# Performance work log

Measured on AMD Instinct MI355X. Metric: run time of the kernel, lower is better.

The kernel has to match this reference:

```python
import jax, jax.numpy as jnp
import numpy as np

HIDDEN = 1024
INNER = 2048  # hidden * expand_factor
STATE = 64
K = 4  # conv kernel size
BATCH, SEQ = 2, 2048


def setup_inputs() -> dict:
    key = jax.random.key(0)
    ks = jax.random.split(key, 8)
    def w(k, shape, scale=0.02):
        return (jax.random.normal(k, shape, jnp.float32) * scale)
    return {
        "x": jax.random.normal(ks[0], (BATCH, SEQ, HIDDEN), jnp.float32),
        "W_in": w(ks[1], (HIDDEN, 2 * INNER)),
        "conv_w": w(ks[2], (INNER, 1, K), 0.2),   # depthwise conv kernel [O, I/groups=1, K]
        "conv_b": jnp.zeros((INNER,), jnp.float32),
        "W_dt": w(ks[3], (INNER, INNER)),
        "b_dt": jnp.linspace(-4.0, -2.0, INNER).astype(jnp.float32),  # log(exp(linspace)) = linspace
        "W_B": w(ks[4], (INNER, STATE)),
        "W_C": w(ks[5], (INNER, STATE)),
        "D": jnp.ones((INNER,), jnp.float32),
        "W_out": w(ks[6], (INNER, HIDDEN)),
    }


def reference(x, W_in, conv_w, conv_b, W_dt, b_dt, W_B, W_C, D, W_out):
    batch, seq_len, _ = x.shape
    inner = W_dt.shape[0]
    state_dim = W_B.shape[1]

    # input projection and gate split
    xz = x @ W_in                              # [B, L, 2*inner]
    x_inner, z = jnp.split(xz, 2, axis=-1)

    # causal depthwise conv1d (pad both sides by K-1 then truncate == left-pad K-1)
    xc = jnp.transpose(x_inner, (0, 2, 1))    # [B, inner, L]
    k = conv_w.shape[-1]
    xc = jax.lax.conv_general_dilated(
        xc, conv_w, window_strides=(1,), padding=[(k - 1, 0)],
        dimension_numbers=("NCH", "OIH", "NCH"), feature_group_count=inner)
    xc = xc + conv_b[None, :, None]
    xc = jax.nn.silu(jnp.transpose(xc, (0, 2, 1)))   # [B, L, inner]

    # selective SSM parameters
    dt = jax.nn.softplus(xc @ W_dt + b_dt)    # [B, L, inner]
    Bm = xc @ W_B                             # [B, L, N]
    Cm = xc @ W_C                             # [B, L, N]
    a = jnp.exp(-dt)                          # [B, L, inner]
    dtx = dt * xc                             # [B, L, inner]

    # sequential selective scan over time: state[B, inner, N]
    def step(state, inp):
        a_t, dtx_t, b_t, c_t = inp
        state = a_t[..., None] * state + dtx_t[..., None] * b_t[:, None, :]
        y_t = jnp.einsum("bin,bn->bi", state, c_t)
        return state, y_t

    init = jnp.zeros((batch, inner, state_dim), x.dtype)
    xs = (jnp.swapaxes(a, 0, 1), jnp.swapaxes(dtx, 0, 1),
          jnp.swapaxes(Bm, 0, 1), jnp.swapaxes(Cm, 0, 1))
    _, ys = jax.lax.scan(step, init, xs)      # ys: [L, B, inner]
    y = jnp.swapaxes(ys, 0, 1) + D * xc       # skip connection

    y = y * jax.nn.silu(z)                    # output gate
    return y @ W_out                          # [B, L, hidden]
```

## Files before the change

### kernel.cpp

```cpp
#include <hip/hip_runtime.h>
#include <hip/hip_bf16.h>
#include <math.h>

#define BATCH  2
#define SEQ    2048
#define HID    1024
#define INNER  2048
#define NSTATE 64
#define NTOK   (BATCH * SEQ)
#define TCHUNK 64
#define NCHUNK (SEQ / TCHUNK)
#define NMID   (INNER + 2 * NSTATE)
#define LDH    1056
#define LDI    2080

typedef __bf16 bf16x8 __attribute__((ext_vector_type(8)));
typedef float  f32x4  __attribute__((ext_vector_type(4)));

typedef const __attribute__((address_space(1))) char* gas_ptr;
typedef __attribute__((address_space(3))) char*       las_ptr;

__device__ __forceinline__ void gload16(const void* g, void* l) {
  __builtin_amdgcn_global_load_lds((gas_ptr)g, (las_ptr)l, 16, 0, 0);
}

__device__ __forceinline__ unsigned short f2bf(float f) {
  __hip_bfloat16 h = __float2bfloat16(f);
  return __builtin_bit_cast(unsigned short, h);
}
__device__ __forceinline__ float bf2f(unsigned short u) {
  unsigned int x = ((unsigned int)u) << 16;
  return __builtin_bit_cast(float, x);
}

__global__ __launch_bounds__(256) void cvt_pad_kernel(
    const float* __restrict__ in, __hip_bfloat16* __restrict__ out, int n4) {
  int i = blockIdx.x * 256 + threadIdx.x;
  if (i >= n4) return;
  const int r = i >> 8;
  const int c = (i & 255) * 4;
  float4 v = *(const float4*)&in[(size_t)r * HID + c];
  ushort4 u;
  u.x = f2bf(v.x); u.y = f2bf(v.y); u.z = f2bf(v.z); u.w = f2bf(v.w);
  *(ushort4*)&out[(size_t)r * LDH + c] = u;
}

__global__ __launch_bounds__(256) void transpose_cvt_kernel(
    const float* __restrict__ in, __hip_bfloat16* __restrict__ out,
    int R, int C, int ostride) {
  __shared__ float tile[32][33];
  int tx = threadIdx.x & 31, ty = threadIdx.x >> 5;
  int c0 = blockIdx.x * 32, r0 = blockIdx.y * 32;
#pragma unroll
  for (int i = 0; i < 4; ++i)
    tile[ty + 8 * i][tx] = in[(size_t)(r0 + ty + 8 * i) * C + c0 + tx];
  __syncthreads();
#pragma unroll
  for (int i = 0; i < 4; ++i)
    out[(size_t)(c0 + ty + 8 * i) * ostride + r0 + tx] =
        __float2bfloat16(tile[tx][ty + 8 * i]);
}

template <int EPI>
__global__ __launch_bounds__(256, 4) void gemm_bt_kernel(
    const __hip_bfloat16* __restrict__ A, const __hip_bfloat16* __restrict__ Bt,
    int M, int N, int Klen, int ldk, int gridN, int nwg, int mnwg,
    float* __restrict__ Cout, int ldc, int ldo,
    __hip_bfloat16* __restrict__ o0, __hip_bfloat16* __restrict__ o1) {
  __shared__ __align__(16) __hip_bfloat16 As[128 * 64];
  __shared__ __align__(16) __hip_bfloat16 Bs[128 * 64];
  const int tid = threadIdx.x;
  const int lane = tid & 63;
  const int w = tid >> 6;
  const int wr = w >> 1, wc = w & 1;

  const int orig = blockIdx.x;
  const int q8 = nwg >> 3, r8 = nwg & 7;
  const int xcd = orig & 7, seq = orig >> 3;
  const int wg = (xcd < r8 ? xcd * (q8 + 1) : r8 * (q8 + 1) + (xcd - r8) * q8) + seq;
  const int kz = wg / mnwg;
  const int wgr = wg - kz * mnwg;
  const int m0 = (wgr / gridN) * 128;
  const int n0 = (wgr % gridN) * 128;

  const __hip_bfloat16* Ab = A + (size_t)kz * Klen;
  const __hip_bfloat16* Bb = Bt + (size_t)kz * Klen;

  f32x4 acc[4][4];
#pragma unroll
  for (int i = 0; i < 4; ++i)
#pragma unroll
    for (int j = 0; j < 4; ++j)
#pragma unroll
      for (int r2 = 0; r2 < 4; ++r2) acc[i][j][r2] = 0.f;

  const int g8row = lane >> 3;
  const int scol = ((lane & 7) ^ g8row) * 8;
  const __hip_bfloat16* Agp = Ab + (size_t)(m0 + w * 32 + g8row) * ldk + scol;
  const __hip_bfloat16* Bgp = Bb + (size_t)(n0 + w * 32 + g8row) * ldk + scol;
  __hip_bfloat16* lA = As + (w * 32) * 64;
  __hip_bfloat16* lB = Bs + (w * 32) * 64;

  const int lrow = lane & 15, lk = lane >> 4;
  const int arow0 = wr * 64 + lrow;
  const int brow0 = wc * 64 + lrow;

  const int nt = Klen >> 6;
  for (int t = 0; t < nt; ++t) {
    __syncthreads();
#pragma unroll
    for (int g = 0; g < 4; ++g) {
      gload16(Agp + (size_t)(g * 8) * ldk + t * 64, lA + (g * 8) * 64);
      gload16(Bgp + (size_t)(g * 8) * ldk + t * 64, lB + (g * 8) * 64);
    }
    __syncthreads();
#pragma unroll
    for (int ss = 0; ss < 2; ++ss) {
      bf16x8 af[4], bv[4];
#pragma unroll
      for (int i = 0; i < 4; ++i) {
        const int ra = arow0 + i * 16;
        af[i] = *(const bf16x8*)(As + ra * 64 + (((ss * 4 + lk) ^ (ra & 7)) * 8));
        const int rb = brow0 + i * 16;
        bv[i] = *(const bf16x8*)(Bs + rb * 64 + (((ss * 4 + lk) ^ (rb & 7)) * 8));
      }
#pragma unroll
      for (int i = 0; i < 4; ++i)
#pragma unroll
        for (int j = 0; j < 4; ++j)
          acc[i][j] = __builtin_amdgcn_mfma_f32_16x16x32_bf16(af[i], bv[j], acc[i][j], 0, 0, 0);
    }
  }

#pragma unroll
  for (int i = 0; i < 4; ++i) {
#pragma unroll
    for (int j = 0; j < 4; ++j) {
#pragma unroll
      for (int r2 = 0; r2 < 4; ++r2) {
        const int row = m0 + wr * 64 + i * 16 + lk * 4 + r2;
        const int col = n0 + wc * 64 + j * 16 + lrow;
        const float v = acc[i][j][r2];
        if constexpr (EPI == 0) {
          Cout[(size_t)kz * M * ldc + (size_t)row * ldc + col] = v;
        } else if constexpr (EPI == 1) {
          if (col < INNER) o0[(size_t)row * ldo + col] = __float2bfloat16(v);
          else             o1[(size_t)row * ldo + (col - INNER)] = __float2bfloat16(v);
        } else {
          o0[(size_t)kz * M * ldc + (size_t)row * ldc + col] = __float2bfloat16(v);
        }
      }
    }
  }
}

__global__ __launch_bounds__(256) void reduce_mid_kernel(
    const __hip_bfloat16* __restrict__ P, const float* __restrict__ bdt,
    const __hip_bfloat16* __restrict__ xch, unsigned int* __restrict__ dtx,
    float* __restrict__ Bm, float* __restrict__ Cm) {
  const int i = blockIdx.x * 256 + threadIdx.x;
  const int row = i / (NMID / 4);
  const int c4 = i - row * (NMID / 4);
  const int col = c4 * 4;
  float4 v = make_float4(0.f, 0.f, 0.f, 0.f);
#pragma unroll
  for (int pp = 0; pp < 2; ++pp) {
    const ushort4 u = *(const ushort4*)&P[(size_t)pp * NTOK * NMID + (size_t)row * NMID + col];
    v.x += bf2f(u.x); v.y += bf2f(u.y); v.z += bf2f(u.z); v.w += bf2f(u.w);
  }
  if (col < INNER) {
    float4 bb = *(const float4*)&bdt[col];
    float4 d;
    d.x = v.x + bb.x; d.y = v.y + bb.y; d.z = v.z + bb.z; d.w = v.w + bb.w;
    d.x = (d.x > 15.f) ? d.x : log1pf(__expf(d.x));
    d.y = (d.y > 15.f) ? d.y : log1pf(__expf(d.y));
    d.z = (d.z > 15.f) ? d.z : log1pf(__expf(d.z));
    d.w = (d.w > 15.f) ? d.w : log1pf(__expf(d.w));
    ushort4 xv = *(const ushort4*)&xch[(size_t)row * LDI + col];
    uint4 o;
    o.x = (unsigned int)f2bf(d.x) | ((unsigned int)xv.x << 16);
    o.y = (unsigned int)f2bf(d.y) | ((unsigned int)xv.y << 16);
    o.z = (unsigned int)f2bf(d.z) | ((unsigned int)xv.z << 16);
    o.w = (unsigned int)f2bf(d.w) | ((unsigned int)xv.w << 16);
    *(uint4*)&dtx[(size_t)row * LDI + col] = o;
  } else if (col < INNER + NSTATE) {
    *(float4*)&Bm[(size_t)row * NSTATE + (col - INNER)] = v;
  } else {
    *(float4*)&Cm[(size_t)row * NSTATE + (col - INNER - NSTATE)] = v;
  }
}

__global__ __launch_bounds__(256) void reduce4b_kernel(
    const __hip_bfloat16* __restrict__ P, float* __restrict__ out, int n4) {
  int i = blockIdx.x * 256 + threadIdx.x;
  if (i >= n4) return;
  float4 acc = make_float4(0.f, 0.f, 0.f, 0.f);
#pragma unroll
  for (int pp = 0; pp < 4; ++pp) {
    ushort4 u = ((const ushort4*)P)[(size_t)pp * n4 + i];
    acc.x += bf2f(u.x); acc.y += bf2f(u.y); acc.z += bf2f(u.z); acc.w += bf2f(u.w);
  }
  ((float4*)out)[i] = acc;
}

__global__ __launch_bounds__(256) void conv_silu_kernel(
    const __hip_bfloat16* __restrict__ xin, const float* __restrict__ cw,
    const float* __restrict__ cb, __hip_bfloat16* __restrict__ xch) {
  int idx = blockIdx.x * 256 + threadIdx.x;
  int cg = idx & 511;
  int tok = idx >> 9;
  int c = cg * 4;
  int l = tok & (SEQ - 1);
  float wv[4][4];
#pragma unroll
  for (int i = 0; i < 4; ++i) {
    float4 w = *(const float4*)&cw[(c + i) * 4];
    wv[i][0] = w.x; wv[i][1] = w.y; wv[i][2] = w.z; wv[i][3] = w.w;
  }
  float4 bias = *(const float4*)&cb[c];
  float r0 = bias.x, r1 = bias.y, r2 = bias.z, r3 = bias.w;
#pragma unroll
  for (int k = 0; k < 4; ++k) {
    const int d = 3 - k;
    if (l >= d) {
      ushort4 xv = *(const ushort4*)&xin[(size_t)(tok - d) * LDI + c];
      r0 = fmaf(bf2f(xv.x), wv[0][k], r0);
      r1 = fmaf(bf2f(xv.y), wv[1][k], r1);
      r2 = fmaf(bf2f(xv.z), wv[2][k], r2);
      r3 = fmaf(bf2f(xv.w), wv[3][k], r3);
    }
  }
  r0 = r0 / (1.f + __expf(-r0));
  r1 = r1 / (1.f + __expf(-r1));
  r2 = r2 / (1.f + __expf(-r2));
  r3 = r3 / (1.f + __expf(-r3));
  ushort4 u;
  u.x = f2bf(r0); u.y = f2bf(r1); u.z = f2bf(r2); u.w = f2bf(r3);
  *(ushort4*)&xch[(size_t)tok * LDI + c] = u;
}

__global__ __launch_bounds__(256) void cumv_kernel(
    const unsigned int* __restrict__ dtx, unsigned short* __restrict__ cumA,
    unsigned int* __restrict__ wT) {
  const int bk = blockIdx.y;
  const int c = blockIdx.x * 256 + threadIdx.x;
  const int b = bk >> 5, k = bk & 31;
  const size_t tokbase = (size_t)(b * SEQ + k * TCHUNK);
  float cum = 1.f;
  unsigned int wreg[32];
#pragma unroll
  for (int t = 0; t < TCHUNK; ++t) {
    const unsigned int pk = dtx[(tokbase + t) * LDI + c];
    const float dtv = bf2f((unsigned short)(pk & 0xffffu));
    const float xc = bf2f((unsigned short)(pk >> 16));
    cum *= __expf(-dtv);
    cum = fmaxf(cum, 1e-30f);
    cumA[(tokbase + t) * INNER + c] = f2bf(cum);
    const unsigned short wb = f2bf(dtv * xc / cum);
    if (t & 1) wreg[t >> 1] |= ((unsigned int)wb) << 16;
    else       wreg[t >> 1] = (unsigned int)wb;
  }
  uint4* dst = (uint4*)(wT + ((size_t)bk * INNER + c) * 32);
#pragma unroll
  for (int j = 0; j < 8; ++j)
    dst[j] = make_uint4(wreg[4 * j], wreg[4 * j + 1], wreg[4 * j + 2], wreg[4 * j + 3]);
}

__global__ __launch_bounds__(256) void chunkG_kernel(
    const float* __restrict__ Bm, const float* __restrict__ Cm,
    __hip_bfloat16* __restrict__ Abuf, __hip_bfloat16* __restrict__ BtBuf) {
  __shared__ float Bsh[TCHUNK][NSTATE + 4];
  __shared__ float Csh[TCHUNK][NSTATE + 4];
  const int bk = blockIdx.x;
  const int b = bk >> 5, k = bk & 31;
  const int tid = threadIdx.x;
  const size_t tokbase = (size_t)(b * SEQ + k * TCHUNK);
  for (int i = tid; i < TCHUNK * 16; i += 256) {
    const int row = i >> 4, q = i & 15;
    *(float4*)&Bsh[row][q * 4] = *(const float4*)&Bm[(tokbase + row) * NSTATE + q * 4];
    *(float4*)&Csh[row][q * 4] = *(const float4*)&Cm[(tokbase + row) * NSTATE + q * 4];
  }
  __syncthreads();
  for (int e = tid; e < 64 * 64; e += 256) {
    const int t = e >> 6, tau = e & 63;
    float g = 0.f;
    if (tau <= t) {
#pragma unroll
      for (int q = 0; q < 16; ++q) {
        const float4 cv = *(const float4*)&Csh[t][q * 4];
        const float4 bv = *(const float4*)&Bsh[tau][q * 4];
        g += cv.x * bv.x + cv.y * bv.y + cv.z * bv.z + cv.w * bv.w;
      }
    }
    Abuf[((size_t)bk * 64 + t) * 128 + tau] = __float2bfloat16(g);
  }
  for (int e = tid; e < 64 * 64; e += 256) {
    const int n2 = e >> 6, r = e & 63;
    BtBuf[((size_t)bk * 64 + n2) * 64 + r] = __float2bfloat16(Bsh[r][n2]);
    Abuf[((size_t)bk * 64 + n2) * 128 + 64 + r] = __float2bfloat16(Csh[n2][r]);
  }
}

__global__ __launch_bounds__(256, 4) void sloc_gemm_kernel(
    const __hip_bfloat16* __restrict__ wT, const __hip_bfloat16* __restrict__ BtBuf,
    const unsigned short* __restrict__ cumA, unsigned short* __restrict__ S) {
  __shared__ __align__(16) __hip_bfloat16 As[128 * 64];
  __shared__ __align__(16) __hip_bfloat16 Bs[64 * 64];
  const int tid = threadIdx.x;
  const int lane = tid & 63;
  const int w = tid >> 6;
  const int bk = blockIdx.x >> 4;
  const int ct = blockIdx.x & 15;
  const int b = bk >> 5, k = bk & 31;
  const int c0 = ct * 128;

  const int g8row = lane >> 3;
  const int scol = ((lane & 7) ^ g8row) * 8;
  const __hip_bfloat16* Ag = wT + ((size_t)bk * INNER + c0 + w * 32 + g8row) * 64 + scol;
  const __hip_bfloat16* Bg = BtBuf + ((size_t)bk * 64 + w * 16 + g8row) * 64 + scol;
  __hip_bfloat16* lA = As + (w * 32) * 64;
  __hip_bfloat16* lB = Bs + (w * 16) * 64;
#pragma unroll
  for (int g = 0; g < 4; ++g) gload16(Ag + (size_t)(g * 8) * 64, lA + (g * 8) * 64);
#pragma unroll
  for (int g = 0; g < 2; ++g) gload16(Bg + (size_t)(g * 8) * 64, lB + (g * 8) * 64);
  __syncthreads();

  const int lrow = lane & 15, lk = lane >> 4;
  f32x4 acc[2][4];
#pragma unroll
  for (int i = 0; i < 2; ++i)
#pragma unroll
    for (int j = 0; j < 4; ++j)
#pragma unroll
      for (int r2 = 0; r2 < 4; ++r2) acc[i][j][r2] = 0.f;

#pragma unroll
  for (int ss = 0; ss < 2; ++ss) {
    bf16x8 af[2], bv[4];
#pragma unroll
    for (int i = 0; i < 2; ++i) {
      const int ra = w * 32 + i * 16 + lrow;
      af[i] = *(const bf16x8*)(As + ra * 64 + (((ss * 4 + lk) ^ (ra & 7)) * 8));
    }
#pragma unroll
    for (int j = 0; j < 4; ++j) {
      const int rb = j * 16 + lrow;
      bv[j] = *(const bf16x8*)(Bs + rb * 64 + (((ss * 4 + lk) ^ (rb & 7)) * 8));
    }
#pragma unroll
    for (int i = 0; i < 2; ++i)
#pragma unroll
      for (int j = 0; j < 4; ++j)
        acc[i][j] = __builtin_amdgcn_mfma_f32_16x16x32_bf16(af[i], bv[j], acc[i][j], 0, 0, 0);
  }

  const size_t tokT = (size_t)(b * SEQ + k * TCHUNK + 63);
#pragma unroll
  for (int i = 0; i < 2; ++i) {
#pragma unroll
    for (int j = 0; j < 4; ++j) {
#pragma unroll
      for (int r2 = 0; r2 < 4; ++r2) {
        const int c = c0 + w * 32 + i * 16 + lk * 4 + r2;
        const int n = j * 16 + lrow;
        const float sc = bf2f(cumA[tokT * INNER + c]);
        S[((size_t)bk * INNER + c) * 64 + n] = f2bf(acc[i][j][r2] * sc);
      }
    }
  }
}

__global__ __launch_bounds__(256) void scan_combine_kernel(
    unsigned short* __restrict__ S, const unsigned short* __restrict__ cumA) {
  const int idx = blockIdx.x * 256 + threadIdx.x;
  const int n = idx & 63;
  const int c = (idx >> 6) & (INNER - 1);
  const int b = idx >> 17;
  float s = 0.f;
  for (int k = 0; k < NCHUNK; ++k) {
    const size_t cs = (size_t)(b * NCHUNK + k) * INNER + c;
    const size_t off = cs * 64 + n;
    const float loc = bf2f(S[off]);
    S[off] = f2bf(s);
    const float ak = bf2f(cumA[((size_t)(b * SEQ + k * TCHUNK + 63)) * INNER + c]);
    s = fmaf(ak, s, loc);
  }
}

__global__ __launch_bounds__(256, 4) void ypre_gemm_kernel(
    const __hip_bfloat16* __restrict__ Abuf, const __hip_bfloat16* __restrict__ wT,
    const unsigned short* __restrict__ S, const unsigned short* __restrict__ cumA,
    const __hip_bfloat16* __restrict__ xch, const __hip_bfloat16* __restrict__ zbf,
    const float* __restrict__ Dv, __hip_bfloat16* __restrict__ ygated) {
  __shared__ __align__(16) __hip_bfloat16 Asm[64 * 128];
  __shared__ __align__(16) __hip_bfloat16 Bsm[128 * 128];
  const int tid = threadIdx.x;
  const int lane = tid & 63;
  const int w = tid >> 6;
  const int bk = blockIdx.x >> 4;
  const int ct = blockIdx.x & 15;
  const int b = bk >> 5, k = bk & 31;
  const int c0 = ct * 128;

  {
#pragma unroll
    for (int g = 0; g < 4; ++g) {
      const int base = w * 16 + g * 4;
      const int col16s = (lane & 15) ^ ((base + (lane >> 4)) & 7);
      const __hip_bfloat16* src =
          Abuf + ((size_t)bk * 64 + base + (lane >> 4)) * 128 + col16s * 8;
      gload16(src, (char*)Asm + base * 256);
    }
  }
  {
    const int row = tid & 127, part = tid >> 7;
    const int c = c0 + row;
    if (part == 0) {
      const uint4* src = (const uint4*)(wT + ((size_t)bk * INNER + c) * 64);
#pragma unroll
      for (int s2 = 0; s2 < 8; ++s2) {
        uint4 v = src[s2];
        *(uint4*)((char*)Bsm + row * 256 + (s2 ^ (row & 7)) * 16) = v;
      }
    } else {
      const uint4* srcS = (const uint4*)(S + ((size_t)bk * INNER + c) * 64);
#pragma unroll
      for (int s2 = 0; s2 < 8; ++s2) {
        uint4 v = srcS[s2];
        *(uint4*)((char*)Bsm + row * 256 + ((8 + s2) ^ (row & 7)) * 16) = v;
      }
    }
  }
  __syncthreads();

  const int lrow = lane & 15, lk = lane >> 4;
  f32x4 acc[8];
#pragma unroll
  for (int j = 0; j < 8; ++j)
#pragma unroll
    for (int r2 = 0; r2 < 4; ++r2) acc[j][r2] = 0.f;

  const int ra = w * 16 + lrow;
#pragma unroll
  for (int kk = 0; kk < 4; ++kk) {
    const int csa = (kk * 4 + lk) ^ (ra & 7);
    bf16x8 af = *(const bf16x8*)((const char*)Asm + ra * 256 + csa * 16);
#pragma unroll
    for (int j = 0; j < 8; ++j) {
      const int rb = j * 16 + lrow;
      const int csb = (kk * 4 + lk) ^ (rb & 7);
      bf16x8 bv = *(const bf16x8*)((const char*)Bsm + rb * 256 + csb * 16);
      acc[j] = __builtin_amdgcn_mfma_f32_16x16x32_bf16(af, bv, acc[j], 0, 0, 0);
    }
  }

  const size_t tokb = (size_t)(b * SEQ + k * TCHUNK);
#pragma unroll
  for (int j = 0; j < 8; ++j) {
#pragma unroll
    for (int r2 = 0; r2 < 4; ++r2) {
      const int t = w * 16 + lk * 4 + r2;
      const int c = c0 + j * 16 + lrow;
      const size_t tok = tokb + t;
      const float ca = bf2f(cumA[tok * INNER + c]);
      const float xc = bf2f(*(const unsigned short*)&xch[tok * LDI + c]);
      const float z = bf2f(*(const unsigned short*)&zbf[tok * LDI + c]);
      const float yt = ca * acc[j][r2] + Dv[c] * xc;
      const float g = z / (1.f + __expf(-z));
      *(unsigned short*)&ygated[tok * LDI + c] = f2bf(yt * g);
    }
  }
}

extern "C" void kernel_launch(void* const* d_in, const int* in_sizes, int n_in,
                              void* d_out, int out_size, void* d_ws, size_t ws_size,
                              hipStream_t stream) {
  const float* x      = (const float*)d_in[0];
  const float* W_in   = (const float*)d_in[1];
  const float* conv_w = (const float*)d_in[2];
  const float* conv_b = (const float*)d_in[3];
  const float* W_dt   = (const float*)d_in[4];
  const float* b_dt   = (const float*)d_in[5];
  const float* W_B    = (const float*)d_in[6];
  const float* W_C    = (const float*)d_in[7];
  const float* Dvec   = (const float*)d_in[8];
  const float* W_out  = (const float*)d_in[9];
  float* out = (float*)d_out;

  char* p = (char*)d_ws;
  auto alloc = [&](size_t bytes) {
    char* r = p;
    p += (bytes + 255) & ~(size_t)255;
    return r;
  };
  __hip_bfloat16* xin   = (__hip_bfloat16*)alloc((size_t)NTOK * LDI * 2);
  __hip_bfloat16* zbf   = (__hip_bfloat16*)alloc((size_t)NTOK * LDI * 2);
  char*           scr   = alloc((size_t)NTOK * LDH * 2 + (size_t)2 * INNER * LDH * 2);
  __hip_bfloat16* WmidT = (__hip_bfloat16*)alloc((size_t)NMID * LDI * 2);
  __hip_bfloat16* WoutT = (__hip_bfloat16*)alloc((size_t)HID * LDI * 2);
  unsigned int*   dtx   = (unsigned int*)alloc((size_t)NTOK * LDI * 4);
  float*          Bm    = (float*)alloc((size_t)NTOK * NSTATE * 4);
  float*          Cm    = (float*)alloc((size_t)NTOK * NSTATE * 4);
  unsigned short* cumA  = (unsigned short*)alloc((size_t)NTOK * INNER * 2);
  __hip_bfloat16* wT    = (__hip_bfloat16*)alloc((size_t)BATCH * NCHUNK * INNER * TCHUNK * 2);
  __hip_bfloat16* Abuf  = (__hip_bfloat16*)alloc((size_t)BATCH * NCHUNK * 64 * 128 * 2);
  __hip_bfloat16* BtBuf = (__hip_bfloat16*)alloc((size_t)BATCH * NCHUNK * 64 * 64 * 2);
  __hip_bfloat16* Pmid  = (__hip_bfloat16*)alloc((size_t)2 * NTOK * NMID * 2);

  __hip_bfloat16* x_bf   = (__hip_bfloat16*)scr;
  __hip_bfloat16* WinT   = (__hip_bfloat16*)(scr + (size_t)NTOK * LDH * 2);
  __hip_bfloat16* xch    = (__hip_bfloat16*)scr;
  __hip_bfloat16* ygated = xin;
  unsigned short* S      = (unsigned short*)Pmid;
  __hip_bfloat16* Pout   = Pmid;

  cvt_pad_kernel<<<(NTOK * HID / 4 + 255) / 256, 256, 0, stream>>>(x, x_bf, NTOK * HID / 4);
  transpose_cvt_kernel<<<dim3((2 * INNER) / 32, HID / 32), 256, 0, stream>>>(W_in, WinT, HID, 2 * INNER, LDH);
  transpose_cvt_kernel<<<dim3(INNER / 32, INNER / 32), 256, 0, stream>>>(W_dt, WmidT, INNER, INNER, LDI);
  transpose_cvt_kernel<<<dim3(NSTATE / 32, INNER / 32), 256, 0, stream>>>(
      W_B, WmidT + (size_t)INNER * LDI, INNER, NSTATE, LDI);
  transpose_cvt_kernel<<<dim3(NSTATE / 32, INNER / 32), 256, 0, stream>>>(
      W_C, WmidT + (size_t)(INNER + NSTATE) * LDI, INNER, NSTATE, LDI);
  transpose_cvt_kernel<<<dim3(HID / 32, INNER / 32), 256, 0, stream>>>(W_out, WoutT, INNER, HID, LDI);

  {
    const int gridN = (2 * INNER) / 128, nwg = (NTOK / 128) * gridN;
    gemm_bt_kernel<1><<<nwg, 256, 0, stream>>>(
        x_bf, WinT, NTOK, 2 * INNER, HID, LDH, gridN, nwg, nwg, nullptr, 0, LDI, xin, zbf);
  }

  conv_silu_kernel<<<(NTOK * (INNER / 4)) / 256, 256, 0, stream>>>(xin, conv_w, conv_b, xch);

  {
    const int gridN = NMID / 128;
    const int mnwg = (NTOK / 128) * gridN;
    const int nwg = mnwg * 2;
    gemm_bt_kernel<2><<<nwg, 256, 0, stream>>>(
        xch, WmidT, NTOK, NMID, INNER / 2, LDI, gridN, nwg, mnwg, nullptr, NMID, 0,
        Pmid, nullptr);
    reduce_mid_kernel<<<(NTOK * (NMID / 4)) / 256, 256, 0, stream>>>(Pmid, b_dt, xch, dtx, Bm, Cm);
  }

  cumv_kernel<<<dim3(INNER / 256, BATCH * NCHUNK), 256, 0, stream>>>(dtx, cumA, (unsigned int*)wT);
  chunkG_kernel<<<BATCH * NCHUNK, 256, 0, stream>>>(Bm, Cm, Abuf, BtBuf);
  sloc_gemm_kernel<<<BATCH * NCHUNK * 16, 256, 0, stream>>>(wT, BtBuf, cumA, S);
  scan_combine_kernel<<<(BATCH * INNER * NSTATE) / 256, 256, 0, stream>>>(S, cumA);
  ypre_gemm_kernel<<<BATCH * NCHUNK * 16, 256, 0, stream>>>(
      Abuf, wT, S, cumA, xch, zbf, Dvec, ygated);

  {
    const int gridN = HID / 128;
    const int mnwg = (NTOK / 128) * gridN;
    const int nwg = mnwg * 4;
    gemm_bt_kernel<2><<<nwg, 256, 0, stream>>>(
        ygated, WoutT, NTOK, HID, INNER / 4, LDI, gridN, nwg, mnwg, nullptr, HID, 0,
        Pout, nullptr);
    const int n4 = NTOK * HID / 4;
    reduce4b_kernel<<<(n4 + 255) / 256, 256, 0, stream>>>(Pout, out, n4);
  }
}
```

Before: 308.6 us.

## Fuse split-K mid reduction and softplus into cumv and chunkG kernels

Removes the reduce_mid kernel and its dtx/Bm/Cm intermediates. cumv now reads both split-K partials and xch directly, applies bias and softplus, and double-buffers its loads in groups of eight. chunkG sums the B/C partials itself and is split four ways per chunk for more parallelism. This saves a kernel launch and a round trip through global memory, at the cost of strided 2-byte loads in cumv and redundant B loads across the four chunkG blocks.

Result: slower. 361.7 us (+17.2%).

```diff
diff --git a/kernel.cpp b/kernel.cpp
--- a/kernel.cpp
+++ b/kernel.cpp
@@ -154,42 +154,6 @@
   }
 }
 
-__global__ __launch_bounds__(256) void reduce_mid_kernel(
-    const __hip_bfloat16* __restrict__ P, const float* __restrict__ bdt,
-    const __hip_bfloat16* __restrict__ xch, unsigned int* __restrict__ dtx,
-    float* __restrict__ Bm, float* __restrict__ Cm) {
-  const int i = blockIdx.x * 256 + threadIdx.x;
-  const int row = i / (NMID / 4);
-  const int c4 = i - row * (NMID / 4);
-  const int col = c4 * 4;
-  float4 v = make_float4(0.f, 0.f, 0.f, 0.f);
-#pragma unroll
-  for (int pp = 0; pp < 2; ++pp) {
-    const ushort4 u = *(const ushort4*)&P[(size_t)pp * NTOK * NMID + (size_t)row * NMID + col];
-    v.x += bf2f(u.x); v.y += bf2f(u.y); v.z += bf2f(u.z); v.w += bf2f(u.w);
-  }
-  if (col < INNER) {
-    float4 bb = *(const float4*)&bdt[col];
-    float4 d;
-    d.x = v.x + bb.x; d.y = v.y + bb.y; d.z = v.z + bb.z; d.w = v.w + bb.w;
-    d.x = (d.x > 15.f) ? d.x : log1pf(__expf(d.x));
-    d.y = (d.y > 15.f) ? d.y : log1pf(__expf(d.y));
-    d.z = (d.z > 15.f) ? d.z : log1pf(__expf(d.z));
-    d.w = (d.w > 15.f) ? d.w : log1pf(__expf(d.w));
-    ushort4 xv = *(const ushort4*)&xch[(size_t)row * LDI + col];
-    uint4 o;
-    o.x = (unsigned int)f2bf(d.x) | ((unsigned int)xv.x << 16);
-    o.y = (unsigned int)f2bf(d.y) | ((unsigned int)xv.y << 16);
-    o.z = (unsigned int)f2bf(d.z) | ((unsigned int)xv.z << 16);
-    o.w = (unsigned int)f2bf(d.w) | ((unsigned int)xv.w << 16);
-    *(uint4*)&dtx[(size_t)row * LDI + col] = o;
-  } else if (col < INNER + NSTATE) {
-    *(float4*)&Bm[(size_t)row * NSTATE + (col - INNER)] = v;
-  } else {
-    *(float4*)&Cm[(size_t)row * NSTATE + (col - INNER - NSTATE)] = v;
-  }
-}
-
 __global__ __launch_bounds__(256) void reduce4b_kernel(
     const __hip_bfloat16* __restrict__ P, float* __restrict__ out, int n4) {
   int i = blockIdx.x * 256 + threadIdx.x;
@@ -240,26 +204,63 @@
 }
 
 __global__ __launch_bounds__(256) void cumv_kernel(
-    const unsigned int* __restrict__ dtx, unsigned short* __restrict__ cumA,
-    unsigned int* __restrict__ wT) {
+    const __hip_bfloat16* __restrict__ P, const float* __restrict__ bdt,
+    const __hip_bfloat16* __restrict__ xch,
+    unsigned short* __restrict__ cumA, unsigned int* __restrict__ wT) {
   const int bk = blockIdx.y;
   const int c = blockIdx.x * 256 + threadIdx.x;
   const int b = bk >> 5, k = bk & 31;
   const size_t tokbase = (size_t)(b * SEQ + k * TCHUNK);
+  const float bb = bdt[c];
+  const unsigned short* P0 = (const unsigned short*)P;
+  const unsigned short* P1 = (const unsigned short*)P + (size_t)NTOK * NMID;
+  const unsigned short* XC = (const unsigned short*)xch;
+
+  float p0a[8], p1a[8], xca[8], p0b[8], p1b[8], xcb[8];
+#define LOADB(tb, A0, A1, A2)                              \
+  do {                                                     \
+    _Pragma("unroll")                                      \
+    for (int j = 0; j < 8; ++j) {                          \
+      const size_t row = tokbase + (tb) + j;               \
+      A0[j] = bf2f(P0[row * NMID + c]);                    \
+      A1[j] = bf2f(P1[row * NMID + c]);                    \
+      A2[j] = bf2f(XC[row * LDI + c]);                     \
+    }                                                      \
+  } while (0)
+
   float cum = 1.f;
   unsigned int wreg[32];
-#pragma unroll
-  for (int t = 0; t < TCHUNK; ++t) {
-    const unsigned int pk = dtx[(tokbase + t) * LDI + c];
-    const float dtv = bf2f((unsigned short)(pk & 0xffffu));
-    const float xc = bf2f((unsigned short)(pk >> 16));
-    cum *= __expf(-dtv);
-    cum = fmaxf(cum, 1e-30f);
-    cumA[(tokbase + t) * INNER + c] = f2bf(cum);
-    const unsigned short wb = f2bf(dtv * xc / cum);
-    if (t & 1) wreg[t >> 1] |= ((unsigned int)wb) << 16;
-    else       wreg[t >> 1] = (unsigned int)wb;
-  }
+  LOADB(0, p0a, p1a, xca);
+#pragma unroll
+  for (int tb = 0; tb < 64; tb += 16) {
+    LOADB(tb + 8, p0b, p1b, xcb);
+#pragma unroll
+    for (int j = 0; j < 8; ++j) {
+      const int t = tb + j;
+      const float dpre = p0a[j] + p1a[j] + bb;
+      const float dtv = (dpre > 15.f) ? dpre : log1pf(__expf(dpre));
+      cum *= __expf(-dtv);
+      cum = fmaxf(cum, 1e-30f);
+      cumA[(tokbase + t) * INNER + c] = f2bf(cum);
+      const unsigned short wb = f2bf(dtv * xca[j] / cum);
+      if (t & 1) wreg[t >> 1] |= ((unsigned int)wb) << 16;
+      else       wreg[t >> 1] = (unsigned int)wb;
+    }
+    if (tb + 16 < 64) LOADB(tb + 16, p0a, p1a, xca);
+#pragma unroll
+    for (int j = 0; j < 8; ++j) {
+      const int t = tb + 8 + j;
+      const float dpre = p0b[j] + p1b[j] + bb;
+      const float dtv = (dpre > 15.f) ? dpre : log1pf(__expf(dpre));
+      cum *= __expf(-dtv);
+      cum = fmaxf(cum, 1e-30f);
+      cumA[(tokbase + t) * INNER + c] = f2bf(cum);
+      const unsigned short wb = f2bf(dtv * xcb[j] / cum);
+      if (t & 1) wreg[t >> 1] |= ((unsigned int)wb) << 16;
+      else       wreg[t >> 1] = (unsigned int)wb;
+    }
+  }
+#undef LOADB
   uint4* dst = (uint4*)(wT + ((size_t)bk * INNER + c) * 32);
 #pragma unroll
   for (int j = 0; j < 8; ++j)
@@ -267,37 +268,56 @@
 }
 
 __global__ __launch_bounds__(256) void chunkG_kernel(
-    const float* __restrict__ Bm, const float* __restrict__ Cm,
+    const __hip_bfloat16* __restrict__ P,
     __hip_bfloat16* __restrict__ Abuf, __hip_bfloat16* __restrict__ BtBuf) {
   __shared__ float Bsh[TCHUNK][NSTATE + 4];
-  __shared__ float Csh[TCHUNK][NSTATE + 4];
-  const int bk = blockIdx.x;
+  __shared__ float Csh[16][NSTATE + 4];
+  const int blk = blockIdx.x;
+  const int bk = blk >> 2, qt = blk & 3;
   const int b = bk >> 5, k = bk & 31;
   const int tid = threadIdx.x;
   const size_t tokbase = (size_t)(b * SEQ + k * TCHUNK);
+  const unsigned short* P0 = (const unsigned short*)P;
+  const unsigned short* P1 = (const unsigned short*)P + (size_t)NTOK * NMID;
+
   for (int i = tid; i < TCHUNK * 16; i += 256) {
     const int row = i >> 4, q = i & 15;
-    *(float4*)&Bsh[row][q * 4] = *(const float4*)&Bm[(tokbase + row) * NSTATE + q * 4];
-    *(float4*)&Csh[row][q * 4] = *(const float4*)&Cm[(tokbase + row) * NSTATE + q * 4];
+    const size_t off = (tokbase + row) * NMID + INNER + q * 4;
+    ushort4 u0 = *(const ushort4*)&P0[off];
+    ushort4 u1 = *(const ushort4*)&P1[off];
+    *(float4*)&Bsh[row][q * 4] = make_float4(
+        bf2f(u0.x) + bf2f(u1.x), bf2f(u0.y) + bf2f(u1.y),
+        bf2f(u0.z) + bf2f(u1.z), bf2f(u0.w) + bf2f(u1.w));
+  }
+  for (int i = tid; i < 16 * 16; i += 256) {
+    const int row = i >> 4, q = i & 15;
+    const size_t off = (tokbase + qt * 16 + row) * NMID + INNER + NSTATE + q * 4;
+    ushort4 u0 = *(const ushort4*)&P0[off];
+    ushort4 u1 = *(const ushort4*)&P1[off];
+    *(float4*)&Csh[row][q * 4] = make_float4(
+        bf2f(u0.x) + bf2f(u1.x), bf2f(u0.y) + bf2f(u1.y),
+        bf2f(u0.z) + bf2f(u1.z), bf2f(u0.w) + bf2f(u1.w));
   }
   __syncthreads();
-  for (int e = tid; e < 64 * 64; e += 256) {
-    const int t = e >> 6, tau = e & 63;
+  for (int e = tid; e < 16 * 64; e += 256) {
+    const int tl = e >> 6, tau = e & 63;
+    const int t = qt * 16 + tl;
     float g = 0.f;
     if (tau <= t) {
 #pragma unroll
       for (int q = 0; q < 16; ++q) {
-        const float4 cv = *(const float4*)&Csh[t][q * 4];
+        const float4 cv = *(const float4*)&Csh[tl][q * 4];
         const float4 bv = *(const float4*)&Bsh[tau][q * 4];
         g += cv.x * bv.x + cv.y * bv.y + cv.z * bv.z + cv.w * bv.w;
       }
     }
     Abuf[((size_t)bk * 64 + t) * 128 + tau] = __float2bfloat16(g);
   }
-  for (int e = tid; e < 64 * 64; e += 256) {
-    const int n2 = e >> 6, r = e & 63;
+  for (int e = tid; e < 16 * 64; e += 256) {
+    const int n2l = e >> 6, r = e & 63;
+    const int n2 = qt * 16 + n2l;
     BtBuf[((size_t)bk * 64 + n2) * 64 + r] = __float2bfloat16(Bsh[r][n2]);
-    Abuf[((size_t)bk * 64 + n2) * 128 + 64 + r] = __float2bfloat16(Csh[n2][r]);
+    Abuf[((size_t)bk * 64 + n2) * 128 + 64 + r] = __float2bfloat16(Csh[n2l][r]);
   }
 }
 
@@ -499,9 +519,6 @@
   char*           scr   = alloc((size_t)NTOK * LDH * 2 + (size_t)2 * INNER * LDH * 2);
   __hip_bfloat16* WmidT = (__hip_bfloat16*)alloc((size_t)NMID * LDI * 2);
   __hip_bfloat16* WoutT = (__hip_bfloat16*)alloc((size_t)HID * LDI * 2);
-  unsigned int*   dtx   = (unsigned int*)alloc((size_t)NTOK * LDI * 4);
-  float*          Bm    = (float*)alloc((size_t)NTOK * NSTATE * 4);
-  float*          Cm    = (float*)alloc((size_t)NTOK * NSTATE * 4);
   unsigned short* cumA  = (unsigned short*)alloc((size_t)NTOK * INNER * 2);
   __hip_bfloat16* wT    = (__hip_bfloat16*)alloc((size_t)BATCH * NCHUNK * INNER * TCHUNK * 2);
   __hip_bfloat16* Abuf  = (__hip_bfloat16*)alloc((size_t)BATCH * NCHUNK * 64 * 128 * 2);
@@ -539,11 +556,11 @@
     gemm_bt_kernel<2><<<nwg, 256, 0, stream>>>(
         xch, WmidT, NTOK, NMID, INNER / 2, LDI, gridN, nwg, mnwg, nullptr, NMID, 0,
         Pmid, nullptr);
-    reduce_mid_kernel<<<(NTOK * (NMID / 4)) / 256, 256, 0, stream>>>(Pmid, b_dt, xch, dtx, Bm, Cm);
-  }
-
-  cumv_kernel<<<dim3(INNER / 256, BATCH * NCHUNK), 256, 0, stream>>>(dtx, cumA, (unsigned int*)wT);
-  chunkG_kernel<<<BATCH * NCHUNK, 256, 0, stream>>>(Bm, Cm, Abuf, BtBuf);
+  }
+
+  cumv_kernel<<<dim3(INNER / 256, BATCH * NCHUNK), 256, 0, stream>>>(
+      Pmid, b_dt, xch, cumA, (unsigned int*)wT);
+  chunkG_kernel<<<BATCH * NCHUNK * 4, 256, 0, stream>>>(Pmid, Abuf, BtBuf);
   sloc_gemm_kernel<<<BATCH * NCHUNK * 16, 256, 0, stream>>>(wT, BtBuf, cumA, S);
   scan_combine_kernel<<<(BATCH * INNER * NSTATE) / 256, 256, 0, stream>>>(S, cumA);
   ypre_gemm_kernel<<<BATCH * NCHUNK * 16, 256, 0, stream>>>(
```
